# Performance work log

Measured on AMD Instinct MI355X. Metric: run time of the kernel, lower is better.

The kernel has to match this reference:

```python
import jax, jax.numpy as jnp
import numpy as np

DT = 0.02        # time step
DT_SKIP = DT * 20
ITERS = 49       # BDF2 iterations hardcoded in forward()
P = 64           # tronc (reduced dim)
NG_U = 8000      # HR sample count, u-equation
NG_V = 8000      # HR sample count, v-equation
B = 32           # batch of trajectories


def setup_inputs() -> dict:
    key = jax.random.key(0)
    k0, k1, k2, k3, k4 = jax.random.split(key, 5)
    state = jax.random.normal(k0, (B, P), dtype=jnp.float32)
    Ap = jax.random.normal(k1, (P, P), dtype=jnp.float32) * 0.05
    W_all_u = jax.random.normal(k2, (4 * NG_U, P), dtype=jnp.float32) * 0.02
    W_all_v = jax.random.normal(k3, (4 * NG_V, P), dtype=jnp.float32) * 0.02
    P_proj = jax.random.normal(k4, (P, NG_U + NG_V), dtype=jnp.float32) * 0.02
    return {"state": state, "Ap": Ap, "W_all_u": W_all_u,
            "W_all_v": W_all_v, "P_proj": P_proj}


def _rhs(a, W_all_u, W_all_v, P_proj):
    # a: (B, p) -> (B, p). Batched hyper-reduced quadratic RHS.
    zu = a @ W_all_u.T                       # (B, 4*Ng_u)
    uu, vu, dxu, dyu = jnp.split(zu, 4, axis=1)
    fu = uu * dxu + vu * dyu                 # (B, Ng_u)
    zv = a @ W_all_v.T                       # (B, 4*Ng_v)
    uv, vv, dxv, dyv = jnp.split(zv, 4, axis=1)
    fv = uv * dxv + vv * dyv                 # (B, Ng_v)
    concat = jnp.concatenate([fu, fv], axis=1)  # (B, Ng_u+Ng_v)
    return -(concat @ P_proj.T)              # (B, p)


def reference(state, Ap, W_all_u, W_all_v, P_proj):
    dt = jnp.float32(DT)
    a0 = state[:, :P]                        # state_rom (B, p)
    eye = jnp.eye(P, dtype=state.dtype)
    mat_1st = eye - dt * Ap[:P, :P]          # I - dt*A
    mat_2nd = 3.0 * eye - 2.0 * dt * Ap[:P, :P]

    # first step: implicit Euler
    f0 = _rhs(a0, W_all_u, W_all_v, P_proj)
    r0 = a0 + dt * f0
    a1 = jnp.linalg.solve(mat_1st, r0.T).T   # == lu_solve(LU_1st, ...)

    # BDF2 recurrence
    def step(carry, _):
        a_prev, f_prev, a_new = carry
        f_new = _rhs(a_new, W_all_u, W_all_v, P_proj)
        r = 4.0 * a_new - a_prev + 4.0 * dt * f_new - 2.0 * dt * f_prev
        a_next = jnp.linalg.solve(mat_2nd, r.T).T
        return (a_new, f_new, a_next), None

    (_, _, out_new), _ = jax.lax.scan(step, (a0, f0, a1), None, length=ITERS)
    return (out_new - a0) / jnp.float32(DT_SKIP)
```

## Files before the change

kernel.cpp:

```cpp
#include <hip/hip_runtime.h>

#define DTC 0.02f
#define INV_DT_SKIP 2.5f
#define NBLK 64
#define NSTEP 50
#define NACT 500

typedef __attribute__((ext_vector_type(8))) __bf16 bf16x8;
typedef __attribute__((ext_vector_type(4))) float f32x4;
typedef __attribute__((ext_vector_type(8))) unsigned short us8;
typedef unsigned long long u64t;

__device__ inline unsigned short f2bf(float x) {
    unsigned u = __float_as_uint(x);
    unsigned r = u + 0x7FFF + ((u >> 16) & 1u);
    return (unsigned short)(r >> 16);
}
__device__ inline float bf2f(unsigned short h) {
    return __uint_as_float(((unsigned)h) << 16);
}
__device__ inline unsigned pack2(float a, float b) {
    return (unsigned)f2bf(a) | ((unsigned)f2bf(b) << 16);
}
__device__ inline void gstore32(unsigned* p, unsigned v) {
    __hip_atomic_store(p, v, __ATOMIC_RELAXED, __HIP_MEMORY_SCOPE_AGENT);
}
__device__ inline unsigned gload32(const unsigned* p) {
    return __hip_atomic_load(p, __ATOMIC_RELAXED, __HIP_MEMORY_SCOPE_AGENT);
}
__device__ inline u64t gload64(const u64t* p) {
    return __hip_atomic_load(p, __ATOMIC_RELAXED, __HIP_MEMORY_SCOPE_AGENT);
}

__global__ __launch_bounds__(256) void kinv(const float* __restrict__ Ap,
                                            float* __restrict__ inv1,
                                            float* __restrict__ inv2) {
    const int t = threadIdx.x;
    const float coef  = (blockIdx.x == 0) ? DTC : (2.0f * DTC / 3.0f);
    const float scale = (blockIdx.x == 0) ? 1.0f : (1.0f / 3.0f);
    float* outp = (blockIdx.x == 0) ? inv1 : inv2;

    __shared__ float ET[64 * 68];
    __shared__ float XA[64 * 68];
    __shared__ float XB[64 * 68];

    for (int idx = t; idx < 4096; idx += 256) {
        int r = idx >> 6, c = idx & 63;
        float e = coef * Ap[idx];
        ET[c * 68 + r] = e;
        XA[r * 68 + c] = ((r == c) ? 1.0f : 0.0f) + e;
    }
    __syncthreads();

    const int rr = (t >> 4) << 2;
    const int cc = (t & 15) << 2;
    float* bufs[2] = {XA, XB};
    for (int it = 0; it < 3; it++) {
        const float* Xin = bufs[it & 1];
        float* Xout = bufs[(it + 1) & 1];
        float acc[4][4];
        #pragma unroll
        for (int i = 0; i < 4; i++)
            #pragma unroll
            for (int j = 0; j < 4; j++)
                acc[i][j] = ((rr + i) == (cc + j)) ? 1.0f : 0.0f;
        for (int k = 0; k < 64; k++) {
            float4 e4 = *(const float4*)&ET[k * 68 + rr];
            float4 x4 = *(const float4*)&Xin[k * 68 + cc];
            float ev[4] = {e4.x, e4.y, e4.z, e4.w};
            float xv[4] = {x4.x, x4.y, x4.z, x4.w};
            #pragma unroll
            for (int i = 0; i < 4; i++)
                #pragma unroll
                for (int j = 0; j < 4; j++)
                    acc[i][j] += ev[i] * xv[j];
        }
        __syncthreads();
        #pragma unroll
        for (int i = 0; i < 4; i++)
            #pragma unroll
            for (int j = 0; j < 4; j++)
                Xout[(rr + i) * 68 + cc + j] = acc[i][j];
        __syncthreads();
    }
    const float* Xf = bufs[1];
    for (int idx = t; idx < 4096; idx += 256) {
        int r = idx >> 6, c = idx & 63;
        outp[idx] = scale * Xf[r * 68 + c];
    }
}

__global__ void kzero(unsigned* __restrict__ flags) {
    if (threadIdx.x < NBLK) flags[threadIdx.x] = 0u;
}

__device__ inline void flagbar(unsigned* flags, int blk, unsigned target) {
    __syncthreads();
    if (threadIdx.x < 64) {
        if (threadIdx.x == 0)
            __hip_atomic_store(&flags[blk], target, __ATOMIC_RELEASE, __HIP_MEMORY_SCOPE_AGENT);
        for (;;) {
            unsigned v = __hip_atomic_load(&flags[threadIdx.x], __ATOMIC_ACQUIRE,
                                           __HIP_MEMORY_SCOPE_AGENT);
            if (__all(v >= target)) break;
            __builtin_amdgcn_s_sleep(2);
        }
    }
    __syncthreads();
}

__global__ __launch_bounds__(512, 2)
void kmain(const float* __restrict__ state,
           const float* __restrict__ Wu,
           const float* __restrict__ Wv,
           const float* __restrict__ Pp,
           const float* __restrict__ inv1,
           const float* __restrict__ inv2,
           unsigned* __restrict__ pbuf,
           unsigned* __restrict__ flags,
           float* __restrict__ out) {
    const int t = threadIdx.x;
    const int l = t & 63;
    const int w = t >> 6;
    const int blk = blockIdx.x;
    const int q = blk * 8 + w;
    const bool active = (q < NACT);

    __shared__ float Ab[3][2176];
    __shared__ float fb[8][2][16][36];
    __shared__ float red[8][1024];
    __shared__ float rbuf[32 * 68];

    for (int i = t; i < 2048; i += 512) Ab[0][(i >> 6) * 68 + (i & 63)] = state[i];
    for (int i = t; i < 8192; i += 512) ((float*)red)[i] = 0.f;

    const int nr = l & 15;
    const int c0 = (l >> 4) << 3;
    const float* W = (q < 250) ? Wu : Wv;
    const int gl0 = ((q < 250) ? q : q - 250) * 32;

    bf16x8 wf[2][4][2], pf[4], sf[4][2];
    if (active) {
        #pragma unroll
        for (int th = 0; th < 2; th++)
            #pragma unroll
            for (int rb = 0; rb < 4; rb++)
                #pragma unroll
                for (int kt = 0; kt < 2; kt++) {
                    const float* s = W + (size_t)(rb * 8000 + gl0 + th * 16 + nr) * 64 + kt * 32 + c0;
                    us8 o;
                    #pragma unroll
                    for (int j = 0; j < 8; j++) o[j] = f2bf(s[j]);
                    wf[th][rb][kt] = __builtin_bit_cast(bf16x8, o);
                }
        #pragma unroll
        for (int pt = 0; pt < 4; pt++) {
            const float* s = Pp + (size_t)(pt * 16 + nr) * 16000 + q * 32 + c0;
            us8 o;
            #pragma unroll
            for (int j = 0; j < 8; j++) o[j] = f2bf(s[j]);
            pf[pt] = __builtin_bit_cast(bf16x8, o);
        }
    }
    if (w < 2) {
        #pragma unroll
        for (int pt = 0; pt < 4; pt++)
            #pragma unroll
            for (int kt = 0; kt < 2; kt++) {
                int p = pt * 16 + nr;
                const float* s = inv2 + (size_t)p * 64 + kt * 32 + c0;
                us8 o;
                #pragma unroll
                for (int j = 0; j < 8; j++) {
                    float v = s[j] - ((p == kt * 32 + c0 + j) ? (1.0f / 3.0f) : 0.0f);
                    o[j] = f2bf(v);
                }
                sf[pt][kt] = __builtin_bit_cast(bf16x8, o);
            }
    }
    __syncthreads();

    int ia_prev = 2, ia_cur = 0, ia_next = 1;
    float fprev[4];

    for (int k = 0; k < NSTEP; k++) {
        const int par = k & 1;
        unsigned* pslot = pbuf + (size_t)par * (NBLK * 1024) + blk * 1024;

        if (active) {
            bf16x8 ahi[2][2], alo[2][2];
            const float* ac = Ab[ia_cur];
            #pragma unroll
            for (int mt = 0; mt < 2; mt++)
                #pragma unroll
                for (int kt = 0; kt < 2; kt++) {
                    us8 hv, lv;
                    #pragma unroll
                    for (int j = 0; j < 8; j++) {
                        float x = ac[(mt * 16 + nr) * 68 + kt * 32 + c0 + j];
                        unsigned short h = f2bf(x);
                        hv[j] = h;
                        lv[j] = f2bf(x - bf2f(h));
                    }
                    ahi[mt][kt] = __builtin_bit_cast(bf16x8, hv);
                    alo[mt][kt] = __builtin_bit_cast(bf16x8, lv);
                }
            const int col = l & 15, q4 = l >> 4;
            #pragma unroll
            for (int mt = 0; mt < 2; mt++)
                #pragma unroll
                for (int th = 0; th < 2; th++) {
                    f32x4 z[4];
                    #pragma unroll
                    for (int rb = 0; rb < 4; rb++) {
                        f32x4 acc = {0.f, 0.f, 0.f, 0.f};
                        #pragma unroll
                        for (int kt = 0; kt < 2; kt++) {
                            acc = __builtin_amdgcn_mfma_f32_16x16x32_bf16(ahi[mt][kt], wf[th][rb][kt], acc, 0, 0, 0);
                            acc = __builtin_amdgcn_mfma_f32_16x16x32_bf16(alo[mt][kt], wf[th][rb][kt], acc, 0, 0, 0);
                        }
                        z[rb] = acc;
                    }
                    #pragma unroll
                    for (int r = 0; r < 4; r++) {
                        float f = z[0][r] * z[2][r] + z[1][r] * z[3][r];
                        fb[w][mt][q4 * 4 + r][th * 16 + col] = f;
                    }
                }
        }
        __syncthreads();

        bf16x8 ff[2];
        if (active) {
            #pragma unroll
            for (int mt = 0; mt < 2; mt++) {
                us8 fv;
                #pragma unroll
                for (int j = 0; j < 8; j++) fv[j] = f2bf(fb[w][mt][nr][c0 + j]);
                ff[mt] = __builtin_bit_cast(bf16x8, fv);
            }
        }

        #pragma unroll
        for (int mt = 0; mt < 2; mt++) {
            if (active) {
                const int col = l & 15, q4 = l >> 4;
                #pragma unroll
                for (int pt = 0; pt < 4; pt++) {
                    f32x4 rc = {0.f, 0.f, 0.f, 0.f};
                    rc = __builtin_amdgcn_mfma_f32_16x16x32_bf16(ff[mt], pf[pt], rc, 0, 0, 0);
                    #pragma unroll
                    for (int r = 0; r < 4; r++)
                        red[w][(q4 * 4 + r) * 64 + pt * 16 + col] = rc[r];
                }
            }
            __syncthreads();
            {
                float s0 = 0.f, s1 = 0.f;
                #pragma unroll
                for (int w8 = 0; w8 < 8; w8++) {
                    s0 += red[w8][2 * t];
                    s1 += red[w8][2 * t + 1];
                }
                gstore32(&pslot[mt * 512 + t], pack2(s0, s1));
            }
            __syncthreads();
        }

        flagbar(flags, blk, (unsigned)(k + 1));

        float fv[4];
        {
            const u64t* pb = (const u64t*)(pbuf + (size_t)par * (NBLK * 1024));
            float s0 = 0.f, s1 = 0.f, s2 = 0.f, s3 = 0.f;
            #pragma unroll 8
            for (int s = 0; s < NBLK; s++) {
                u64t v = gload64(pb + (size_t)s * 512 + t);
                unsigned lo = (unsigned)v, hi = (unsigned)(v >> 32);
                s0 += __uint_as_float(lo << 16);
                s1 += __uint_as_float(lo & 0xffff0000u);
                s2 += __uint_as_float(hi << 16);
                s3 += __uint_as_float(hi & 0xffff0000u);
            }
            fv[0] = -s0; fv[1] = -s1; fv[2] = -s2; fv[3] = -s3;
        }

        {
            const int b = (4 * t) >> 6, p0 = (4 * t) & 63;
            #pragma unroll
            for (int jj = 0; jj < 4; jj++) {
                float f = fv[jj];
                int row = b * 68 + p0 + jj;
                float av = Ab[ia_cur][row];
                float rv = (k == 0) ? (av + DTC * f)
                                    : (4.f * av - Ab[ia_prev][row]
                                       + 4.f * DTC * f - 2.f * DTC * fprev[jj]);
                rbuf[row] = rv;
                fprev[jj] = f;
            }
        }
        __syncthreads();

        if (w < 2) {
            auto solve = [&](const bf16x8 (&S)[4][2], float cbase) {
                int m = w * 16 + nr;
                bf16x8 rhi[2], rlo[2];
                #pragma unroll
                for (int kt = 0; kt < 2; kt++) {
                    us8 hv, lv;
                    #pragma unroll
                    for (int j = 0; j < 8; j++) {
                        float x = rbuf[m * 68 + kt * 32 + c0 + j];
                        unsigned short h = f2bf(x);
                        hv[j] = h;
                        lv[j] = f2bf(x - bf2f(h));
                    }
                    rhi[kt] = __builtin_bit_cast(bf16x8, hv);
                    rlo[kt] = __builtin_bit_cast(bf16x8, lv);
                }
                int col = l & 15, q4 = l >> 4;
                #pragma unroll
                for (int pt = 0; pt < 4; pt++) {
                    f32x4 acc;
                    #pragma unroll
                    for (int r = 0; r < 4; r++)
                        acc[r] = rbuf[(w * 16 + q4 * 4 + r) * 68 + pt * 16 + col] * cbase;
                    #pragma unroll
                    for (int kt = 0; kt < 2; kt++) {
                        acc = __builtin_amdgcn_mfma_f32_16x16x32_bf16(rhi[kt], S[pt][kt], acc, 0, 0, 0);
                        acc = __builtin_amdgcn_mfma_f32_16x16x32_bf16(rlo[kt], S[pt][kt], acc, 0, 0, 0);
                    }
                    #pragma unroll
                    for (int r = 0; r < 4; r++)
                        Ab[ia_next][(w * 16 + q4 * 4 + r) * 68 + pt * 16 + col] = acc[r];
                }
            };
            if (k == 0) {
                bf16x8 s1f[4][2];
                #pragma unroll
                for (int pt = 0; pt < 4; pt++)
                    #pragma unroll
                    for (int kt = 0; kt < 2; kt++) {
                        int p = pt * 16 + nr;
                        const float* s = inv1 + (size_t)p * 64 + kt * 32 + c0;
                        us8 o;
                        #pragma unroll
                        for (int j = 0; j < 8; j++) {
                            float v = s[j] - ((p == kt * 32 + c0 + j) ? 1.0f : 0.0f);
                            o[j] = f2bf(v);
                        }
                        s1f[pt][kt] = __builtin_bit_cast(bf16x8, o);
                    }
                solve(s1f, 1.0f);
            } else {
                solve(sf, 1.0f / 3.0f);
            }
        }
        __syncthreads();

        if (k == NSTEP - 1 && blk == 0) {
            for (int i = t; i < 2048; i += 512)
                out[i] = (Ab[ia_next][(i >> 6) * 68 + (i & 63)] - state[i]) * INV_DT_SKIP;
        }

        int tmp = ia_prev; ia_prev = ia_cur; ia_cur = ia_next; ia_next = tmp;
    }
}

extern "C" void kernel_launch(void* const* d_in, const int* in_sizes, int n_in,
                              void* d_out, int out_size, void* d_ws, size_t ws_size,
                              hipStream_t stream) {
    const float* state = (const float*)d_in[0];
    const float* Ap    = (const float*)d_in[1];
    const float* Wu    = (const float*)d_in[2];
    const float* Wv    = (const float*)d_in[3];
    const float* Pp    = (const float*)d_in[4];
    float* out = (float*)d_out;
    float* ws  = (float*)d_ws;

    float* inv1 = ws;
    float* inv2 = ws + 4096;
    unsigned* flags = (unsigned*)(ws + 8192);
    unsigned* pbuf  = (unsigned*)(ws + 8192 + 64);

    hipLaunchKernelGGL(kzero, dim3(1), dim3(64), 0, stream, flags);
    hipLaunchKernelGGL(kinv, dim3(2), dim3(256), 0, stream, Ap, inv1, inv2);
    hipLaunchKernelGGL(kmain, dim3(NBLK), dim3(512), 0, stream,
                       state, Wu, Wv, Pp, inv1, inv2, pbuf, flags, out);
}
```

Before: 656.1 us.

## Halve persistent block count, give each wave two chunks, spread solve over all waves

Cuts the persistent grid from 64 to 32 blocks. Each active wave now holds weights for two 32-column chunks in registers and accumulates the projection over both chunks before writing its partial. The per-step small solve is spread across all 8 waves, one 16x16 tile each, instead of 2 waves doing 4 tiles each. Fewer blocks shrink the cross-block flag barrier and the global partial-sum reduction. The cost is more register pressure and more serial MFMA work per wave.

```diff
diff --git a/kernel.cpp b/kernel.cpp
--- a/kernel.cpp
+++ b/kernel.cpp
@@ -2,9 +2,8 @@
 
 #define DTC 0.02f
 #define INV_DT_SKIP 2.5f
-#define NBLK 64
+#define NBLK 32
 #define NSTEP 50
-#define NACT 500
 
 typedef __attribute__((ext_vector_type(8))) __bf16 bf16x8;
 typedef __attribute__((ext_vector_type(4))) float f32x4;
@@ -24,9 +23,6 @@
 }
 __device__ inline void gstore32(unsigned* p, unsigned v) {
     __hip_atomic_store(p, v, __ATOMIC_RELAXED, __HIP_MEMORY_SCOPE_AGENT);
-}
-__device__ inline unsigned gload32(const unsigned* p) {
-    return __hip_atomic_load(p, __ATOMIC_RELAXED, __HIP_MEMORY_SCOPE_AGENT);
 }
 __device__ inline u64t gload64(const u64t* p) {
     return __hip_atomic_load(p, __ATOMIC_RELAXED, __HIP_MEMORY_SCOPE_AGENT);
@@ -100,7 +96,7 @@
         if (threadIdx.x == 0)
             __hip_atomic_store(&flags[blk], target, __ATOMIC_RELEASE, __HIP_MEMORY_SCOPE_AGENT);
         for (;;) {
-            unsigned v = __hip_atomic_load(&flags[threadIdx.x], __ATOMIC_ACQUIRE,
+            unsigned v = __hip_atomic_load(&flags[threadIdx.x & (NBLK - 1)], __ATOMIC_ACQUIRE,
                                            __HIP_MEMORY_SCOPE_AGENT);
             if (__all(v >= target)) break;
             __builtin_amdgcn_s_sleep(2);
@@ -123,60 +119,66 @@
     const int l = t & 63;
     const int w = t >> 6;
     const int blk = blockIdx.x;
-    const int q = blk * 8 + w;
-    const bool active = (q < NACT);
+    const int gw = blk * 8 + w;
+    const bool active = (gw < 250);
 
     __shared__ float Ab[3][2176];
-    __shared__ float fb[8][2][16][36];
+    __shared__ float fb[8][16][36];
     __shared__ float red[8][1024];
     __shared__ float rbuf[32 * 68];
 
     for (int i = t; i < 2048; i += 512) Ab[0][(i >> 6) * 68 + (i & 63)] = state[i];
-    for (int i = t; i < 8192; i += 512) ((float*)red)[i] = 0.f;
+    if (!active)
+        for (int i = l; i < 1024; i += 64) red[w][i] = 0.f;
 
     const int nr = l & 15;
     const int c0 = (l >> 4) << 3;
-    const float* W = (q < 250) ? Wu : Wv;
-    const int gl0 = ((q < 250) ? q : q - 250) * 32;
-
-    bf16x8 wf[2][4][2], pf[4], sf[4][2];
+    const int cA = gw * 2;
+    const float* W = (cA < 250) ? Wu : Wv;
+    const int glA = ((cA < 250) ? cA : cA - 250) * 32;
+
+    bf16x8 wf[2][2][4][2], pf[2][4], sfw[2];
     if (active) {
         #pragma unroll
-        for (int th = 0; th < 2; th++)
-            #pragma unroll
-            for (int rb = 0; rb < 4; rb++)
-                #pragma unroll
-                for (int kt = 0; kt < 2; kt++) {
-                    const float* s = W + (size_t)(rb * 8000 + gl0 + th * 16 + nr) * 64 + kt * 32 + c0;
-                    us8 o;
-                    #pragma unroll
-                    for (int j = 0; j < 8; j++) o[j] = f2bf(s[j]);
-                    wf[th][rb][kt] = __builtin_bit_cast(bf16x8, o);
-                }
-        #pragma unroll
-        for (int pt = 0; pt < 4; pt++) {
-            const float* s = Pp + (size_t)(pt * 16 + nr) * 16000 + q * 32 + c0;
+        for (int ch = 0; ch < 2; ch++)
+            #pragma unroll
+            for (int th = 0; th < 2; th++)
+                #pragma unroll
+                for (int rb = 0; rb < 4; rb++)
+                    #pragma unroll
+                    for (int kt = 0; kt < 2; kt++) {
+                        const float* s = W + (size_t)(rb * 8000 + glA + ch * 32 + th * 16 + nr) * 64
+                                           + kt * 32 + c0;
+                        us8 o;
+                        #pragma unroll
+                        for (int j = 0; j < 8; j++) o[j] = f2bf(s[j]);
+                        wf[ch][th][rb][kt] = __builtin_bit_cast(bf16x8, o);
+                    }
+        #pragma unroll
+        for (int ch = 0; ch < 2; ch++)
+            #pragma unroll
+            for (int pt = 0; pt < 4; pt++) {
+                const float* s = Pp + (size_t)(pt * 16 + nr) * 16000 + (cA + ch) * 32 + c0;
+                us8 o;
+                #pragma unroll
+                for (int j = 0; j < 8; j++) o[j] = f2bf(s[j]);
+                pf[ch][pt] = __builtin_bit_cast(bf16x8, o);
+            }
+    }
+    {
+        const int ptS = w & 3;
+        #pragma unroll
+        for (int kt = 0; kt < 2; kt++) {
+            int p = ptS * 16 + nr;
+            const float* s = inv2 + (size_t)p * 64 + kt * 32 + c0;
             us8 o;
             #pragma unroll
-            for (int j = 0; j < 8; j++) o[j] = f2bf(s[j]);
-            pf[pt] = __builtin_bit_cast(bf16x8, o);
-        }
-    }
-    if (w < 2) {
-        #pragma unroll
-        for (int pt = 0; pt < 4; pt++)
-            #pragma unroll
-            for (int kt = 0; kt < 2; kt++) {
-                int p = pt * 16 + nr;
-                const float* s = inv2 + (size_t)p * 64 + kt * 32 + c0;
-                us8 o;
-                #pragma unroll
-                for (int j = 0; j < 8; j++) {
-                    float v = s[j] - ((p == kt * 32 + c0 + j) ? (1.0f / 3.0f) : 0.0f);
-                    o[j] = f2bf(v);
-                }
-                sf[pt][kt] = __builtin_bit_cast(bf16x8, o);
-            }
+            for (int j = 0; j < 8; j++) {
+                float v = s[j] - ((p == kt * 32 + c0 + j) ? (1.0f / 3.0f) : 0.0f);
+                o[j] = f2bf(v);
+            }
+            sfw[kt] = __builtin_bit_cast(bf16x8, o);
+        }
     }
     __syncthreads();
 
@@ -187,72 +189,66 @@
         const int par = k & 1;
         unsigned* pslot = pbuf + (size_t)par * (NBLK * 1024) + blk * 1024;
 
-        if (active) {
-            bf16x8 ahi[2][2], alo[2][2];
-            const float* ac = Ab[ia_cur];
-            #pragma unroll
-            for (int mt = 0; mt < 2; mt++)
-                #pragma unroll
-                for (int kt = 0; kt < 2; kt++) {
-                    us8 hv, lv;
-                    #pragma unroll
-                    for (int j = 0; j < 8; j++) {
-                        float x = ac[(mt * 16 + nr) * 68 + kt * 32 + c0 + j];
-                        unsigned short h = f2bf(x);
-                        hv[j] = h;
-                        lv[j] = f2bf(x - bf2f(h));
-                    }
-                    ahi[mt][kt] = __builtin_bit_cast(bf16x8, hv);
-                    alo[mt][kt] = __builtin_bit_cast(bf16x8, lv);
-                }
-            const int col = l & 15, q4 = l >> 4;
-            #pragma unroll
-            for (int mt = 0; mt < 2; mt++)
-                #pragma unroll
-                for (int th = 0; th < 2; th++) {
-                    f32x4 z[4];
-                    #pragma unroll
-                    for (int rb = 0; rb < 4; rb++) {
-                        f32x4 acc = {0.f, 0.f, 0.f, 0.f};
-                        #pragma unroll
-                        for (int kt = 0; kt < 2; kt++) {
-                            acc = __builtin_amdgcn_mfma_f32_16x16x32_bf16(ahi[mt][kt], wf[th][rb][kt], acc, 0, 0, 0);
-                            acc = __builtin_amdgcn_mfma_f32_16x16x32_bf16(alo[mt][kt], wf[th][rb][kt], acc, 0, 0, 0);
-                        }
-                        z[rb] = acc;
-                    }
-                    #pragma unroll
-                    for (int r = 0; r < 4; r++) {
-                        float f = z[0][r] * z[2][r] + z[1][r] * z[3][r];
-                        fb[w][mt][q4 * 4 + r][th * 16 + col] = f;
-                    }
-                }
-        }
-        __syncthreads();
-
-        bf16x8 ff[2];
-        if (active) {
-            #pragma unroll
-            for (int mt = 0; mt < 2; mt++) {
-                us8 fv;
-                #pragma unroll
-                for (int j = 0; j < 8; j++) fv[j] = f2bf(fb[w][mt][nr][c0 + j]);
-                ff[mt] = __builtin_bit_cast(bf16x8, fv);
-            }
-        }
-
         #pragma unroll
         for (int mt = 0; mt < 2; mt++) {
             if (active) {
+                bf16x8 ahi[2], alo[2];
+                {
+                    const float* ac = Ab[ia_cur];
+                    #pragma unroll
+                    for (int kt = 0; kt < 2; kt++) {
+                        us8 hv, lv;
+                        #pragma unroll
+                        for (int j = 0; j < 8; j++) {
+                            float x = ac[(mt * 16 + nr) * 68 + kt * 32 + c0 + j];
+                            unsigned short h = f2bf(x);
+                            hv[j] = h;
+                            lv[j] = f2bf(x - bf2f(h));
+                        }
+                        ahi[kt] = __builtin_bit_cast(bf16x8, hv);
+                        alo[kt] = __builtin_bit_cast(bf16x8, lv);
+                    }
+                }
                 const int col = l & 15, q4 = l >> 4;
-                #pragma unroll
-                for (int pt = 0; pt < 4; pt++) {
-                    f32x4 rc = {0.f, 0.f, 0.f, 0.f};
-                    rc = __builtin_amdgcn_mfma_f32_16x16x32_bf16(ff[mt], pf[pt], rc, 0, 0, 0);
+                f32x4 racc[4] = {{0.f,0.f,0.f,0.f},{0.f,0.f,0.f,0.f},
+                                 {0.f,0.f,0.f,0.f},{0.f,0.f,0.f,0.f}};
+                #pragma unroll
+                for (int ch = 0; ch < 2; ch++) {
+                    #pragma unroll
+                    for (int th = 0; th < 2; th++) {
+                        f32x4 z[4];
+                        #pragma unroll
+                        for (int rb = 0; rb < 4; rb++) {
+                            f32x4 acc = {0.f, 0.f, 0.f, 0.f};
+                            #pragma unroll
+                            for (int kt = 0; kt < 2; kt++) {
+                                acc = __builtin_amdgcn_mfma_f32_16x16x32_bf16(ahi[kt], wf[ch][th][rb][kt], acc, 0, 0, 0);
+                                acc = __builtin_amdgcn_mfma_f32_16x16x32_bf16(alo[kt], wf[ch][th][rb][kt], acc, 0, 0, 0);
+                            }
+                            z[rb] = acc;
+                        }
+                        #pragma unroll
+                        for (int r = 0; r < 4; r++) {
+                            float f = z[0][r] * z[2][r] + z[1][r] * z[3][r];
+                            fb[w][q4 * 4 + r][th * 16 + col] = f;
+                        }
+                    }
+                    bf16x8 ff;
+                    {
+                        us8 fv8;
+                        #pragma unroll
+                        for (int j = 0; j < 8; j++) fv8[j] = f2bf(fb[w][nr][c0 + j]);
+                        ff = __builtin_bit_cast(bf16x8, fv8);
+                    }
+                    #pragma unroll
+                    for (int pt = 0; pt < 4; pt++)
+                        racc[pt] = __builtin_amdgcn_mfma_f32_16x16x32_bf16(ff, pf[ch][pt], racc[pt], 0, 0, 0);
+                }
+                #pragma unroll
+                for (int pt = 0; pt < 4; pt++)
                     #pragma unroll
                     for (int r = 0; r < 4; r++)
-                        red[w][(q4 * 4 + r) * 64 + pt * 16 + col] = rc[r];
-                }
+                        red[w][(q4 * 4 + r) * 64 + pt * 16 + col] = racc[pt][r];
             }
             __syncthreads();
             {
@@ -273,7 +269,7 @@
         {
             const u64t* pb = (const u64t*)(pbuf + (size_t)par * (NBLK * 1024));
             float s0 = 0.f, s1 = 0.f, s2 = 0.f, s3 = 0.f;
-            #pragma unroll 8
+            #pragma unroll
             for (int s = 0; s < NBLK; s++) {
                 u64t v = gload64(pb + (size_t)s * 512 + t);
                 unsigned lo = (unsigned)v, hi = (unsigned)(v >> 32);
@@ -301,60 +297,55 @@
         }
         __syncthreads();
 
-        if (w < 2) {
-            auto solve = [&](const bf16x8 (&S)[4][2], float cbase) {
-                int m = w * 16 + nr;
-                bf16x8 rhi[2], rlo[2];
+        {
+            const int mtS = w >> 2, ptS = w & 3;
+            const int col = l & 15, q4 = l >> 4;
+            bf16x8 S0, S1;
+            float cb;
+            if (k == 0) {
                 #pragma unroll
                 for (int kt = 0; kt < 2; kt++) {
-                    us8 hv, lv;
+                    int p = ptS * 16 + nr;
+                    const float* s = inv1 + (size_t)p * 64 + kt * 32 + c0;
+                    us8 o;
                     #pragma unroll
                     for (int j = 0; j < 8; j++) {
-                        float x = rbuf[m * 68 + kt * 32 + c0 + j];
-                        unsigned short h = f2bf(x);
-                        hv[j] = h;
-                        lv[j] = f2bf(x - bf2f(h));
-                    }
-                    rhi[kt] = __builtin_bit_cast(bf16x8, hv);
-                    rlo[kt] = __builtin_bit_cast(bf16x8, lv);
-                }
-                int col = l & 15, q4 = l >> 4;
-                #pragma unroll
-                for (int pt = 0; pt < 4; pt++) {
-                    f32x4 acc;
-                    #pragma unroll
-                    for (int r = 0; r < 4; r++)
-                        acc[r] = rbuf[(w * 16 + q4 * 4 + r) * 68 + pt * 16 + col] * cbase;
-                    #pragma unroll
-                    for (int kt = 0; kt < 2; kt++) {
-                        acc = __builtin_amdgcn_mfma_f32_16x16x32_bf16(rhi[kt], S[pt][kt], acc, 0, 0, 0);
-                        acc = __builtin_amdgcn_mfma_f32_16x16x32_bf16(rlo[kt], S[pt][kt], acc, 0, 0, 0);
-                    }
-                    #pragma unroll
-                    for (int r = 0; r < 4; r++)
-                        Ab[ia_next][(w * 16 + q4 * 4 + r) * 68 + pt * 16 + col] = acc[r];
-                }
-            };
-            if (k == 0) {
-                bf16x8 s1f[4][2];
-                #pragma unroll
-                for (int pt = 0; pt < 4; pt++)
-                    #pragma unroll
-                    for (int kt = 0; kt < 2; kt++) {
-                        int p = pt * 16 + nr;
-                        const float* s = inv1 + (size_t)p * 64 + kt * 32 + c0;
-                        us8 o;
-                        #pragma unroll
-                        for (int j = 0; j < 8; j++) {
-                            float v = s[j] - ((p == kt * 32 + c0 + j) ? 1.0f : 0.0f);
-                            o[j] = f2bf(v);
-                        }
-                        s1f[pt][kt] = __builtin_bit_cast(bf16x8, o);
-                    }
-                solve(s1f, 1.0f);
+                        float v = s[j] - ((p == kt * 32 + c0 + j) ? 1.0f : 0.0f);
+                        o[j] = f2bf(v);
+                    }
+                    if (kt == 0) S0 = __builtin_bit_cast(bf16x8, o);
+                    else         S1 = __builtin_bit_cast(bf16x8, o);
+                }
+                cb = 1.0f;
             } else {
-                solve(sf, 1.0f / 3.0f);
-            }
+                S0 = sfw[0]; S1 = sfw[1];
+                cb = 1.0f / 3.0f;
+            }
+            bf16x8 rhi[2], rlo[2];
+            #pragma unroll
+            for (int kt = 0; kt < 2; kt++) {
+                us8 hv, lv;
+                #pragma unroll
+                for (int j = 0; j < 8; j++) {
+                    float x = rbuf[(mtS * 16 + nr) * 68 + kt * 32 + c0 + j];
+                    unsigned short h = f2bf(x);
+                    hv[j] = h;
+                    lv[j] = f2bf(x - bf2f(h));
+                }
+                rhi[kt] = __builtin_bit_cast(bf16x8, hv);
+                rlo[kt] = __builtin_bit_cast(bf16x8, lv);
+            }
+            f32x4 acc;
+            #pragma unroll
+            for (int r = 0; r < 4; r++)
+                acc[r] = rbuf[(mtS * 16 + q4 * 4 + r) * 68 + ptS * 16 + col] * cb;
+            acc = __builtin_amdgcn_mfma_f32_16x16x32_bf16(rhi[0], S0, acc, 0, 0, 0);
+            acc = __builtin_amdgcn_mfma_f32_16x16x32_bf16(rlo[0], S0, acc, 0, 0, 0);
+            acc = __builtin_amdgcn_mfma_f32_16x16x32_bf16(rhi[1], S1, acc, 0, 0, 0);
+            acc = __builtin_amdgcn_mfma_f32_16x16x32_bf16(rlo[1], S1, acc, 0, 0, 0);
+            #pragma unroll
+            for (int r = 0; r < 4; r++)
+                Ab[ia_next][(mtS * 16 + q4 * 4 + r) * 68 + ptS * 16 + col] = acc[r];
         }
         __syncthreads();
 
```

New measurement: 613.1 us. 1.07x faster.
